# Optimization experiments

Hardware: AMD Instinct MI355X
Metric: run time of the kernel (lower is better)

Reference implementation:

```python
import jax, jax.numpy as jnp
import numpy as np

NUM_HEADS = 8


def setup_inputs() -> dict:
    key = jax.random.key(0)
    ks = jax.random.split(key, 8)
    B, N, D, H = 4, 1200, 256, NUM_HEADS
    return {
        "query_bbox": jax.random.normal(ks[0], (B, N, 10), jnp.float32) * 20.0,
        "query_feat": jax.random.normal(ks[1], (B, N, D), jnp.float32),
        "beta_w": jax.random.normal(ks[2], (H, D), jnp.float32) * 0.02,
        "beta_b": jax.random.uniform(ks[3], (H,), jnp.float32, 0.0, 2.0),
        "in_proj_w": jax.random.normal(ks[4], (3 * D, D), jnp.float32) * (D ** -0.5),
        "in_proj_b": jnp.zeros((3 * D,), jnp.float32),
        "out_proj_w": jax.random.normal(ks[5], (D, D), jnp.float32) * (D ** -0.5),
        "out_proj_b": jnp.zeros((D,), jnp.float32),
    }


def reference(query_bbox, query_feat, beta_w, beta_b, in_proj_w, in_proj_b,
              out_proj_w, out_proj_b):
    B, N, D = query_feat.shape
    H = NUM_HEADS
    hd = D // H

    # center_dists (no_grad in original): negative pairwise L2 of bbox centers
    centers = jax.lax.stop_gradient(query_bbox[..., :2])            # [B,N,2]
    diff = centers[:, :, None, :] - centers[:, None, :, :]          # [B,N,N,2]
    dist = -jnp.sqrt(jnp.sum(diff * diff, axis=-1))                 # [B,N,N]

    # per-head learned beta scale
    beta = jnp.einsum('bnd,hd->bhn', query_feat, beta_w) + beta_b[None, :, None]  # [B,H,N]
    attn_mask = dist[:, None, :, :] * beta[..., None]               # [B,H,N,N]

    # multi-head self-attention with additive mask
    qkv = jnp.einsum('bnd,ed->bne', query_feat, in_proj_w) + in_proj_b
    q, k, v = jnp.split(qkv, 3, axis=-1)
    q = q.reshape(B, N, H, hd)
    k = k.reshape(B, N, H, hd)
    v = v.reshape(B, N, H, hd)

    scores = jnp.einsum('bqhd,bkhd->bhqk', q, k) * (hd ** -0.5) + attn_mask
    attn = jax.nn.softmax(scores, axis=-1)                          # [B,H,N,N]
    out = jnp.einsum('bhqk,bkhd->bqhd', attn, v).reshape(B, N, D)
    return jnp.einsum('bnd,ed->bne', out, out_proj_w) + out_proj_b
```

## Files before the change

### kernel.cpp

```cpp
#include <hip/hip_runtime.h>
#include <hip/hip_bf16.h>

#define BC 4
#define NQ 1200
#define DIM 256
#define NH 8
#define HD 32
#define E3 768
#define MROWS (BC*NQ)
#define SCALE 0.17677669529663687f
#define L2E 1.4426950408889634f
#define SL2E (SCALE * L2E)

#define VT2_PER_BH 40960
#define VT2_PER_HH 20480

typedef __attribute__((ext_vector_type(8))) short bf16x8;
typedef __attribute__((ext_vector_type(4))) float f32x4;
typedef __attribute__((ext_vector_type(2))) unsigned u32x2;

__device__ inline short f2bf(float f) {
    __hip_bfloat16 h = __float2bfloat16(f);
    return *reinterpret_cast<short*>(&h);
}
__device__ inline unsigned pack2bf(float a, float b) {
    unsigned ua = (unsigned short)f2bf(a);
    unsigned ub = (unsigned short)f2bf(b);
    return ua | (ub << 16);
}

__device__ __forceinline__ void gll16(const void* g, void* l) {
    __builtin_amdgcn_global_load_lds(
        (const __attribute__((address_space(1))) unsigned*)g,
        (__attribute__((address_space(3))) unsigned*)l, 16, 0, 0);
}

__global__ void beta_ctr_kernel(const float* __restrict__ feat, const float* __restrict__ bw,
                                const float* __restrict__ bb, const float* __restrict__ bbox,
                                float* __restrict__ beta, float* __restrict__ ctr) {
    int gw = (blockIdx.x * 256 + threadIdx.x) >> 6;
    int lane = threadIdx.x & 63;
    if (gw >= MROWS) return;
    const float* frow = feat + (size_t)gw * DIM;
    float acc[NH];
#pragma unroll
    for (int h = 0; h < NH; ++h) acc[h] = 0.f;
#pragma unroll
    for (int it = 0; it < DIM / 64; ++it) {
        int d = it * 64 + lane;
        float f = frow[d];
#pragma unroll
        for (int h = 0; h < NH; ++h) acc[h] += f * bw[h * DIM + d];
    }
#pragma unroll
    for (int h = 0; h < NH; ++h) {
#pragma unroll
        for (int off = 32; off; off >>= 1) acc[h] += __shfl_xor(acc[h], off);
    }
    int b = gw / NQ, n = gw % NQ;
#pragma unroll
    for (int h = 0; h < NH; ++h) {
        float v = acc[h] + bb[h];
        if (lane == h) beta[(b * NH + h) * NQ + n] = v;
    }
    if (lane == 0) {
        ctr[gw * 2]     = bbox[(size_t)gw * 10];
        ctr[gw * 2 + 1] = bbox[(size_t)gw * 10 + 1];
    }
}

template<bool AF32, bool BF32, bool OUTF32, bool VTOUT, bool QSCALE>
__global__ __launch_bounds__(256) void gemm_k256(const void* __restrict__ Av,
                                                 const void* __restrict__ Bv,
                                                 const float* __restrict__ bias,
                                                 void* __restrict__ Cout, int Edim,
                                                 short* __restrict__ vtout) {
    __shared__ short as[64][40];
    __shared__ short bs[64][40];
    int m0 = blockIdx.y * 64, e0 = blockIdx.x * 64;
    int t = threadIdx.x, lane = t & 63, wid = t >> 6;
    int wr = (wid >> 1) * 32, wc = (wid & 1) * 32;
    f32x4 acc[2][2] = {};
    int lrow = t >> 2, lch = t & 3;
    const float qs = (QSCALE && e0 < DIM) ? SL2E : 1.f;

    for (int ks = 0; ks < DIM / 32; ++ks) {
        bf16x8 av, wv;
        if (AF32) {
            const float* A = (const float*)Av;
            float4 f0 = *(const float4*)(A + (size_t)(m0 + lrow) * DIM + ks * 32 + lch * 8);
            float4 f1 = *(const float4*)(A + (size_t)(m0 + lrow) * DIM + ks * 32 + lch * 8 + 4);
            av[0]=f2bf(f0.x); av[1]=f2bf(f0.y); av[2]=f2bf(f0.z); av[3]=f2bf(f0.w);
            av[4]=f2bf(f1.x); av[5]=f2bf(f1.y); av[6]=f2bf(f1.z); av[7]=f2bf(f1.w);
        } else {
            av = *(const bf16x8*)((const short*)Av + (size_t)(m0 + lrow) * DIM + ks * 32 + lch * 8);
        }
        if (BF32) {
            const float* B = (const float*)Bv;
            float4 f0 = *(const float4*)(B + (size_t)(e0 + lrow) * DIM + ks * 32 + lch * 8);
            float4 f1 = *(const float4*)(B + (size_t)(e0 + lrow) * DIM + ks * 32 + lch * 8 + 4);
            wv[0]=f2bf(f0.x*qs); wv[1]=f2bf(f0.y*qs); wv[2]=f2bf(f0.z*qs); wv[3]=f2bf(f0.w*qs);
            wv[4]=f2bf(f1.x*qs); wv[5]=f2bf(f1.y*qs); wv[6]=f2bf(f1.z*qs); wv[7]=f2bf(f1.w*qs);
        } else {
            wv = *(const bf16x8*)((const short*)Bv + (size_t)(e0 + lrow) * DIM + ks * 32 + lch * 8);
        }
        __syncthreads();
        *(bf16x8*)&as[lrow][lch * 8] = av;
        *(bf16x8*)&bs[lrow][lch * 8] = wv;
        __syncthreads();
#pragma unroll
        for (int sm = 0; sm < 2; ++sm) {
            bf16x8 af = *(const bf16x8*)&as[wr + sm * 16 + (lane & 15)][(lane >> 4) * 8];
#pragma unroll
            for (int sn = 0; sn < 2; ++sn) {
                bf16x8 bfv = *(const bf16x8*)&bs[wc + sn * 16 + (lane & 15)][(lane >> 4) * 8];
                acc[sm][sn] = __builtin_amdgcn_mfma_f32_16x16x32_bf16(af, bfv, acc[sm][sn], 0, 0, 0);
            }
        }
    }
#pragma unroll
    for (int sm = 0; sm < 2; ++sm)
#pragma unroll
        for (int sn = 0; sn < 2; ++sn) {
            int e = e0 + wc + sn * 16 + (lane & 15);
            float bv = bias[e];
            if (QSCALE && e < DIM) bv *= SL2E;
            float vals[4];
            int mbase = m0 + wr + sm * 16 + (lane >> 4) * 4;
#pragma unroll
            for (int r = 0; r < 4; ++r) vals[r] = acc[sm][sn][r] + bv;
            if (VTOUT && e >= 2 * DIM) {
                int dv = e - 2 * DIM;
                int hv = dv >> 5, dd = dv & 31;
                int hh = dd >> 4, di = dd & 15;
                int bb = mbase / NQ, nn = mbase - bb * NQ;
                short4 o;
                o.x = f2bf(vals[0]); o.y = f2bf(vals[1]);
                o.z = f2bf(vals[2]); o.w = f2bf(vals[3]);
                size_t off = (size_t)(bb * NH + hv) * VT2_PER_BH + hh * VT2_PER_HH
                           + (nn >> 3) * 128 + di * 8 + (nn & 7);
                *(short4*)&vtout[off] = o;
            } else {
#pragma unroll
                for (int r = 0; r < 4; ++r) {
                    int m = mbase + r;
                    if (OUTF32) ((float*)Cout)[(size_t)m * Edim + e] = vals[r];
                    else        ((short*)Cout)[(size_t)m * Edim + e] = f2bf(vals[r]);
                }
            }
        }
}

#define BUFSZ 17408
#define KT_OFF 0
#define VT_OFF 8192
#define CK_OFF 16384
#define PL_OFF (2*BUFSZ)
__global__ __launch_bounds__(256, 4) void attn_kernel(const short* __restrict__ qkv,
                                                      const short* __restrict__ vt2,
                                                      const float* __restrict__ beta,
                                                      const float* __restrict__ ctr,
                                                      short* __restrict__ attnb) {
    __shared__ __align__(16) char smem[2 * BUFSZ + 4096];

    const int t = threadIdx.x, lane = t & 63, w = t >> 6;
    const int g = lane >> 4, i = lane & 15;
    const int qg = w >> 1, ksp = w & 1;
    const int bh = blockIdx.y, b = bh >> 3, h = bh & 7;
    const int q0 = blockIdx.x * 32 + qg * 16;
    const int q = q0 + i, qc = min(q, NQ - 1);
    const int kwb = ksp * 64;
    const int bq = b * NQ;

    bf16x8 qf = *(const bf16x8*)(qkv + (size_t)(bq + qc) * E3 + h * HD + g * 8);
    const float cqx = ctr[(bq + qc) * 2];
    const float cqy = ctr[(bq + qc) * 2 + 1];
    const float nbql = -beta[(b * NH + h) * NQ + qc] * L2E;

    float mcur = 0.f, lsum = 0.f;
    f32x4 o0 = {}, o1 = {};

    const int koff = ((t >> 6) << 4) + (t & 15);
    const short* kld0 = qkv + (size_t)bq * E3 + DIM + h * HD + (size_t)koff * E3 + ((t >> 4) & 3) * 8;
    const short* kld1 = kld0 + (size_t)64 * E3;
    const short* vld0 = vt2 + (size_t)bh * VT2_PER_BH + (((t >> 4) & 15)) * 128 + (t & 15) * 8;
    const short* vld1 = vld0 + VT2_PER_HH;
    const char*  cld  = (const char*)(ctr + (size_t)bq * 2) + lane * 16;

    auto stage_issue = [&](int base) {
        gll16(kld0, &smem[base + KT_OFF + t * 16]);
        gll16(kld1, &smem[base + KT_OFF + (t + 256) * 16]);
        gll16(vld0, &smem[base + VT_OFF + t * 16]);
        gll16(vld1, &smem[base + VT_OFF + (t + 256) * 16]);
        if (w == 0) gll16(cld, &smem[base + CK_OFF + lane * 16]);
        kld0 += (size_t)128 * E3; kld1 += (size_t)128 * E3;
        vld0 += 2048; vld1 += 2048; cld += 1024;
    };

    stage_issue(0);
    __syncthreads();
    int cur = 0;

    for (int kb = 0; kb < NQ; kb += 128) {
        const bool haveNext = (kb + 128 < NQ);
        const bool tail = (kb + 128 > NQ);
        if (haveNext) stage_issue((cur ^ 1) * BUFSZ);

        const int cb = cur * BUFSZ;
        float st[16];
        f32x4 cinit = {-mcur, -mcur, -mcur, -mcur};
#pragma unroll
        for (int kcl = 0; kcl < 4; ++kcl) {
            bf16x8 af = *(const bf16x8*)&smem[cb + KT_OFF + (((ksp * 4 + kcl) * 64 + lane) << 4)];
            f32x4 s = __builtin_amdgcn_mfma_f32_16x16x32_bf16(af, qf, cinit, 0, 0, 0);
            int lk = kwb + kcl * 16 + 4 * g;
            float4 cA = *(const float4*)&smem[cb + CK_OFF + lk * 8];
            float4 cB = *(const float4*)&smem[cb + CK_OFF + lk * 8 + 16];
            float cxv[4] = {cA.x, cA.z, cB.x, cB.z};
            float cyv[4] = {cA.y, cA.w, cB.y, cB.w};
#pragma unroll
            for (int r = 0; r < 4; ++r) {
                float dx = cqx - cxv[r], dy = cqy - cyv[r];
                float d2 = __builtin_fmaf(dx, dx, dy * dy);
                float dist = __builtin_amdgcn_sqrtf(d2);
                st[kcl * 4 + r] = __builtin_fmaf(dist, nbql, s[r]);
            }
            if (tail) {
#pragma unroll
                for (int r = 0; r < 4; ++r)
                    if (kb + lk + r >= NQ) st[kcl * 4 + r] = -1e30f;
            }
        }

        float a0 = fmaxf(fmaxf(st[0],  st[1]),  st[2]);
        float a1 = fmaxf(fmaxf(st[3],  st[4]),  st[5]);
        float a2 = fmaxf(fmaxf(st[6],  st[7]),  st[8]);
        float a3 = fmaxf(fmaxf(st[9],  st[10]), st[11]);
        float a4 = fmaxf(fmaxf(st[12], st[13]), st[14]);
        float vm = fmaxf(fmaxf(fmaxf(a0, a1), a2), fmaxf(fmaxf(a3, a4), st[15]));
        if (!__all(vm <= 8.0f)) {
            float vr = fmaxf(vm, __shfl_xor(vm, 16));
            vr = fmaxf(vr, __shfl_xor(vr, 32));
            float dm = fmaxf(vr, 0.f);
            float al = __builtin_amdgcn_exp2f(-dm);
            mcur += dm;
            lsum *= al;
#pragma unroll
            for (int r = 0; r < 4; ++r) { o0[r] *= al; o1[r] *= al; }
#pragma unroll
            for (int x = 0; x < 16; ++x) st[x] -= dm;
        }
#pragma unroll
        for (int x = 0; x < 16; ++x) st[x] = __builtin_amdgcn_exp2f(st[x]);
        float s0 = (st[0] + st[1]) + (st[2] + st[3]);
        float s1 = (st[4] + st[5]) + (st[6] + st[7]);
        float s2 = (st[8] + st[9]) + (st[10] + st[11]);
        float s3 = (st[12] + st[13]) + (st[14] + st[15]);
        lsum += (s0 + s1) + (s2 + s3);

#pragma unroll
        for (int kc2 = 0; kc2 < 2; ++kc2) {
#pragma unroll
            for (int kk = 0; kk < 2; ++kk) {
                int kcl = 2 * kc2 + kk;
                u32x2 pw = {pack2bf(st[kcl * 4 + 0], st[kcl * 4 + 1]),
                            pack2bf(st[kcl * 4 + 2], st[kcl * 4 + 3])};
                *(u32x2*)&smem[PL_OFF + (w << 10) + (((kk << 1) + (g >> 1)) << 8) + (i << 4) + ((g & 1) << 3)] = pw;
            }
            bf16x8 pbf = *(const bf16x8*)&smem[PL_OFF + (w << 10) + (g << 8) + (i << 4)];
            int vidx = (8 * ksp + 4 * kc2 + g) * 16 + i;
            bf16x8 vf0 = *(const bf16x8*)&smem[cb + VT_OFF + (vidx << 4)];
            bf16x8 vf1 = *(const bf16x8*)&smem[cb + VT_OFF + ((256 + vidx) << 4)];
            o0 = __builtin_amdgcn_mfma_f32_16x16x32_bf16(vf0, pbf, o0, 0, 0, 0);
            o1 = __builtin_amdgcn_mfma_f32_16x16x32_bf16(vf1, pbf, o1, 0, 0, 0);
        }

        __syncthreads();
        cur ^= 1;
    }

    lsum += __shfl_xor(lsum, 16);
    lsum += __shfl_xor(lsum, 32);
    float* mrg = (float*)smem;
    float* my = mrg + (w * 64 + lane) * 10;
    my[0] = mcur; my[1] = lsum;
#pragma unroll
    for (int r = 0; r < 4; ++r) { my[2 + r] = o0[r]; my[6 + r] = o1[r]; }
    __syncthreads();
    const float* pr = mrg + ((w ^ 1) * 64 + lane) * 10;
    float m2 = pr[0], l2 = pr[1];
    float mN = fmaxf(mcur, m2);
    float a1 = __builtin_amdgcn_exp2f(mcur - mN);
    float a2 = __builtin_amdgcn_exp2f(m2 - mN);
    float inv = 1.f / (lsum * a1 + l2 * a2);
    int hh = w & 1;
    f32x4 mine = hh ? o1 : o0;
    if (q < NQ) {
        short4 outv;
        float vals[4];
#pragma unroll
        for (int r = 0; r < 4; ++r) vals[r] = (mine[r] * a1 + pr[2 + hh * 4 + r] * a2) * inv;
        outv.x = f2bf(vals[0]); outv.y = f2bf(vals[1]);
        outv.z = f2bf(vals[2]); outv.w = f2bf(vals[3]);
        *(short4*)&attnb[(size_t)(bq + q) * DIM + h * HD + hh * 16 + 4 * g] = outv;
    }
}

extern "C" void kernel_launch(void* const* d_in, const int* in_sizes, int n_in,
                              void* d_out, int out_size, void* d_ws, size_t ws_size,
                              hipStream_t stream) {
    const float* bbox  = (const float*)d_in[0];
    const float* feat  = (const float*)d_in[1];
    const float* bw    = (const float*)d_in[2];
    const float* bb    = (const float*)d_in[3];
    const float* in_w  = (const float*)d_in[4];
    const float* in_b  = (const float*)d_in[5];
    const float* out_w = (const float*)d_in[6];
    const float* out_b = (const float*)d_in[7];
    float* out = (float*)d_out;

    char* ws = (char*)d_ws;
    size_t off = 0;
    auto alloc = [&](size_t bytes) { void* p = ws + off; off += (bytes + 255) & ~255ull; return p; };
    short* qkvb  = (short*)alloc((size_t)MROWS * E3 * 2);
    short* vtb   = (short*)alloc((size_t)BC * NH * VT2_PER_BH * 2);
    short* attnb = (short*)alloc((size_t)MROWS * DIM * 2);
    float* betab = (float*)alloc((size_t)BC * NH * NQ * 4);
    float* ctr   = (float*)alloc((size_t)BC * NQ * 2 * 4 + 1024);
    (void)ws_size; (void)in_sizes; (void)n_in; (void)out_size;

    beta_ctr_kernel<<<MROWS / 4, 256, 0, stream>>>(feat, bw, bb, bbox, betab, ctr);
    gemm_k256<true, true, false, true, true><<<dim3(E3 / 64, MROWS / 64), 256, 0, stream>>>(feat, in_w, in_b, qkvb, E3, vtb);
    attn_kernel<<<dim3((NQ + 31) / 32, BC * NH), 256, 0, stream>>>(qkvb, vtb, betab, ctr, attnb);
    gemm_k256<false, true, true, false, false><<<dim3(DIM / 64, MROWS / 64), 256, 0, stream>>>(attnb, out_w, out_b, out, DIM, nullptr);
}
```

Measured before the change: 61.86 us.

## Use hardware packed bf16 convert and compute softmax row sums via MFMA

Replaces the software float-to-bf16 conversions with the v_cvt_pk_bf16_f32 instruction in the GEMM, V-transpose and attention output paths. In the attention loop, the per-lane row-sum of exponentials and its cross-lane shuffle reduction are replaced by an extra MFMA against an all-ones bf16 vector. That moves the softmax denominator onto the matrix unit, and the sum is now taken over the bf16-rounded probabilities, which matches what the PV product uses. MFMA issue is also wrapped in s_setprio to favour the matrix work, at the cost of one more MFMA per chunk.

```diff
diff --git a/kernel.cpp b/kernel.cpp
--- a/kernel.cpp
+++ b/kernel.cpp
@@ -18,15 +18,16 @@
 typedef __attribute__((ext_vector_type(8))) short bf16x8;
 typedef __attribute__((ext_vector_type(4))) float f32x4;
 typedef __attribute__((ext_vector_type(2))) unsigned u32x2;
+typedef __attribute__((ext_vector_type(4))) unsigned u32x4;
 
 __device__ inline short f2bf(float f) {
     __hip_bfloat16 h = __float2bfloat16(f);
     return *reinterpret_cast<short*>(&h);
 }
-__device__ inline unsigned pack2bf(float a, float b) {
-    unsigned ua = (unsigned short)f2bf(a);
-    unsigned ub = (unsigned short)f2bf(b);
-    return ua | (ub << 16);
+__device__ __forceinline__ unsigned cvtpk(float lo, float hi) {
+    unsigned r;
+    asm("v_cvt_pk_bf16_f32 %0, %1, %2" : "=v"(r) : "v"(lo), "v"(hi));
+    return r;
 }
 
 __device__ __forceinline__ void gll16(const void* g, void* l) {
@@ -90,8 +91,9 @@
             const float* A = (const float*)Av;
             float4 f0 = *(const float4*)(A + (size_t)(m0 + lrow) * DIM + ks * 32 + lch * 8);
             float4 f1 = *(const float4*)(A + (size_t)(m0 + lrow) * DIM + ks * 32 + lch * 8 + 4);
-            av[0]=f2bf(f0.x); av[1]=f2bf(f0.y); av[2]=f2bf(f0.z); av[3]=f2bf(f0.w);
-            av[4]=f2bf(f1.x); av[5]=f2bf(f1.y); av[6]=f2bf(f1.z); av[7]=f2bf(f1.w);
+            u32x4 p = {cvtpk(f0.x, f0.y), cvtpk(f0.z, f0.w),
+                       cvtpk(f1.x, f1.y), cvtpk(f1.z, f1.w)};
+            av = __builtin_bit_cast(bf16x8, p);
         } else {
             av = *(const bf16x8*)((const short*)Av + (size_t)(m0 + lrow) * DIM + ks * 32 + lch * 8);
         }
@@ -99,8 +101,9 @@
             const float* B = (const float*)Bv;
             float4 f0 = *(const float4*)(B + (size_t)(e0 + lrow) * DIM + ks * 32 + lch * 8);
             float4 f1 = *(const float4*)(B + (size_t)(e0 + lrow) * DIM + ks * 32 + lch * 8 + 4);
-            wv[0]=f2bf(f0.x*qs); wv[1]=f2bf(f0.y*qs); wv[2]=f2bf(f0.z*qs); wv[3]=f2bf(f0.w*qs);
-            wv[4]=f2bf(f1.x*qs); wv[5]=f2bf(f1.y*qs); wv[6]=f2bf(f1.z*qs); wv[7]=f2bf(f1.w*qs);
+            u32x4 p = {cvtpk(f0.x * qs, f0.y * qs), cvtpk(f0.z * qs, f0.w * qs),
+                       cvtpk(f1.x * qs, f1.y * qs), cvtpk(f1.z * qs, f1.w * qs)};
+            wv = __builtin_bit_cast(bf16x8, p);
         } else {
             wv = *(const bf16x8*)((const short*)Bv + (size_t)(e0 + lrow) * DIM + ks * 32 + lch * 8);
         }
@@ -134,12 +137,10 @@
                 int hv = dv >> 5, dd = dv & 31;
                 int hh = dd >> 4, di = dd & 15;
                 int bb = mbase / NQ, nn = mbase - bb * NQ;
-                short4 o;
-                o.x = f2bf(vals[0]); o.y = f2bf(vals[1]);
-                o.z = f2bf(vals[2]); o.w = f2bf(vals[3]);
+                u32x2 o = {cvtpk(vals[0], vals[1]), cvtpk(vals[2], vals[3])};
                 size_t off = (size_t)(bb * NH + hv) * VT2_PER_BH + hh * VT2_PER_HH
                            + (nn >> 3) * 128 + di * 8 + (nn & 7);
-                *(short4*)&vtout[off] = o;
+                *(u32x2*)&vtout[off] = o;
             } else {
 #pragma unroll
                 for (int r = 0; r < 4; ++r) {
@@ -177,8 +178,11 @@
     const float cqy = ctr[(bq + qc) * 2 + 1];
     const float nbql = -beta[(b * NH + h) * NQ + qc] * L2E;
 
-    float mcur = 0.f, lsum = 0.f;
-    f32x4 o0 = {}, o1 = {};
+    const short onebf = (short)0x3F80;
+    const bf16x8 ones = {onebf, onebf, onebf, onebf, onebf, onebf, onebf, onebf};
+
+    float mcur = 0.f;
+    f32x4 o0 = {}, o1 = {}, oS = {};
 
     const int koff = ((t >> 6) << 4) + (t & 15);
     const short* kld0 = qkv + (size_t)bq * E3 + DIM + h * HD + (size_t)koff * E3 + ((t >> 4) & 3) * 8;
@@ -244,43 +248,40 @@
             float dm = fmaxf(vr, 0.f);
             float al = __builtin_amdgcn_exp2f(-dm);
             mcur += dm;
-            lsum *= al;
 #pragma unroll
             for (int r = 0; r < 4; ++r) { o0[r] *= al; o1[r] *= al; }
+            oS[0] *= al;
 #pragma unroll
             for (int x = 0; x < 16; ++x) st[x] -= dm;
         }
 #pragma unroll
         for (int x = 0; x < 16; ++x) st[x] = __builtin_amdgcn_exp2f(st[x]);
-        float s0 = (st[0] + st[1]) + (st[2] + st[3]);
-        float s1 = (st[4] + st[5]) + (st[6] + st[7]);
-        float s2 = (st[8] + st[9]) + (st[10] + st[11]);
-        float s3 = (st[12] + st[13]) + (st[14] + st[15]);
-        lsum += (s0 + s1) + (s2 + s3);
 
 #pragma unroll
         for (int kc2 = 0; kc2 < 2; ++kc2) {
 #pragma unroll
             for (int kk = 0; kk < 2; ++kk) {
                 int kcl = 2 * kc2 + kk;
-                u32x2 pw = {pack2bf(st[kcl * 4 + 0], st[kcl * 4 + 1]),
-                            pack2bf(st[kcl * 4 + 2], st[kcl * 4 + 3])};
+                u32x2 pw = {cvtpk(st[kcl * 4 + 0], st[kcl * 4 + 1]),
+                            cvtpk(st[kcl * 4 + 2], st[kcl * 4 + 3])};
                 *(u32x2*)&smem[PL_OFF + (w << 10) + (((kk << 1) + (g >> 1)) << 8) + (i << 4) + ((g & 1) << 3)] = pw;
             }
             bf16x8 pbf = *(const bf16x8*)&smem[PL_OFF + (w << 10) + (g << 8) + (i << 4)];
             int vidx = (8 * ksp + 4 * kc2 + g) * 16 + i;
             bf16x8 vf0 = *(const bf16x8*)&smem[cb + VT_OFF + (vidx << 4)];
             bf16x8 vf1 = *(const bf16x8*)&smem[cb + VT_OFF + ((256 + vidx) << 4)];
+            __builtin_amdgcn_s_setprio(1);
             o0 = __builtin_amdgcn_mfma_f32_16x16x32_bf16(vf0, pbf, o0, 0, 0, 0);
             o1 = __builtin_amdgcn_mfma_f32_16x16x32_bf16(vf1, pbf, o1, 0, 0, 0);
+            oS = __builtin_amdgcn_mfma_f32_16x16x32_bf16(ones, pbf, oS, 0, 0, 0);
+            __builtin_amdgcn_s_setprio(0);
         }
 
         __syncthreads();
         cur ^= 1;
     }
 
-    lsum += __shfl_xor(lsum, 16);
-    lsum += __shfl_xor(lsum, 32);
+    float lsum = oS[0];
     float* mrg = (float*)smem;
     float* my = mrg + (w * 64 + lane) * 10;
     my[0] = mcur; my[1] = lsum;
@@ -296,13 +297,11 @@
     int hh = w & 1;
     f32x4 mine = hh ? o1 : o0;
     if (q < NQ) {
-        short4 outv;
         float vals[4];
 #pragma unroll
         for (int r = 0; r < 4; ++r) vals[r] = (mine[r] * a1 + pr[2 + hh * 4 + r] * a2) * inv;
-        outv.x = f2bf(vals[0]); outv.y = f2bf(vals[1]);
-        outv.z = f2bf(vals[2]); outv.w = f2bf(vals[3]);
-        *(short4*)&attnb[(size_t)(bq + q) * DIM + h * HD + hh * 16 + 4 * g] = outv;
+        u32x2 outv = {cvtpk(vals[0], vals[1]), cvtpk(vals[2], vals[3])};
+        *(u32x2*)&attnb[(size_t)(bq + q) * DIM + h * HD + hh * 16 + 4 * g] = outv;
     }
 }
 
```

After: 60.74 us. About the same (-1.8%).
